# Performance work log

Hardware: AMD Instinct MI355X
Metric: run time of the kernel (lower is better)

## Reference

```python
import jax, jax.numpy as jnp
import numpy as np

A_NUM = 9
C_NUM = 20

def setup_inputs() -> dict:
    key = jax.random.key(0)
    ks = jax.random.split(key, 12)
    B, Cin, H, W = 32, 256, 56, 56
    hidden = 256
    N, M = 64, 2048
    out_ch = 5 * A_NUM + C_NUM
    features = jax.random.normal(ks[0], (B, Cin, H, W), jnp.float32)
    w1 = jax.random.normal(ks[1], (hidden, Cin), jnp.float32) * (1.0 / np.sqrt(Cin))
    b1 = jax.random.normal(ks[2], (hidden,), jnp.float32) * 0.01
    w2 = jax.random.normal(ks[3], (out_ch, hidden), jnp.float32) * (1.0 / np.sqrt(hidden))
    b2 = jax.random.normal(ks[4], (out_ch,), jnp.float32) * 0.01
    # anchor shapes (w, h), positive sizes in grid units
    anc = 1.0 + 5.0 * jax.random.uniform(ks[5], (A_NUM, 2), jnp.float32)
    # grid of cell centers
    xs = jnp.arange(W, dtype=jnp.float32) + 0.5
    ys = jnp.arange(H, dtype=jnp.float32) + 0.5
    gx, gy = jnp.meshgrid(xs, ys, indexing='xy')  # (H, W)
    grid = jnp.broadcast_to(jnp.stack([gx, gy], axis=-1)[None], (B, H, W, 2))
    # GT boxes (x1, y1, x2, y2, cls) with x1<x2, y1<y2
    x1 = jax.random.uniform(ks[6], (B, N), jnp.float32) * (W - 9.0)
    y1 = jax.random.uniform(ks[7], (B, N), jnp.float32) * (H - 9.0)
    bw = 1.0 + 7.0 * jax.random.uniform(ks[8], (B, N), jnp.float32)
    bh = 1.0 + 7.0 * jax.random.uniform(ks[9], (B, N), jnp.float32)
    cls = jax.random.randint(ks[10], (B, N), 0, C_NUM).astype(jnp.float32)
    bboxes = jnp.stack([x1, y1, x1 + bw, y1 + bh, cls], axis=-1)
    total_anchors = B * A_NUM * H * W
    pos_anchor_idx = jax.random.randint(ks[11], (M,), 0, total_anchors, jnp.int64 if jax.config.jax_enable_x64 else jnp.int32)
    neg_anchor_idx = jax.random.randint(jax.random.fold_in(key, 99), (M,), 0, total_anchors, jnp.int64 if jax.config.jax_enable_x64 else jnp.int32)
    GT_offsets = jax.random.normal(jax.random.fold_in(key, 100), (M, 4), jnp.float32) * 0.1
    return {"features": features, "w1": w1, "b1": b1, "w2": w2, "b2": b2,
            "anc": anc, "grid": grid, "bboxes": bboxes, "GT_offsets": GT_offsets,
            "pos_anchor_idx": pos_anchor_idx, "neg_anchor_idx": neg_anchor_idx}

def _generate_anchor(anc, grid):
    # grid: (B,H,W,2), anc: (A,2) -> anchors (B,A,H,W,4) as (x1,y1,x2,y2)
    g = grid[:, None]                      # (B,1,H,W,2)
    a = anc[None, :, None, None]           # (1,A,1,1,2)
    return jnp.concatenate([g - a / 2, g + a / 2], axis=-1)

def _generate_proposal_yolo(anchors, offsets):
    ctr = (anchors[..., :2] + anchors[..., 2:]) / 2
    wh = anchors[..., 2:] - anchors[..., :2]
    new_wh = wh * jnp.exp(offsets[..., 2:])
    new_ctr = ctr + offsets[..., :2]
    return jnp.concatenate([new_ctr - new_wh / 2, new_ctr + new_wh / 2], axis=-1)

def _iou(proposals, bboxes):
    # proposals (B,A,H,W,4) -> (B,AHW,4); bboxes (B,N,5) -> iou (B,AHW,N)
    B = proposals.shape[0]
    p = proposals.reshape(B, -1, 4)[:, :, None, :]   # (B,AHW,1,4)
    g = bboxes[:, None, :, :]                        # (B,1,N,5)
    ix1 = jnp.maximum(p[..., 0], g[..., 0])
    iy1 = jnp.maximum(p[..., 1], g[..., 1])
    ix2 = jnp.minimum(p[..., 2], g[..., 2])
    iy2 = jnp.minimum(p[..., 3], g[..., 3])
    inter = jnp.clip(ix2 - ix1, 0) * jnp.clip(iy2 - iy1, 0)
    gt_area = (bboxes[:, :, 2] - bboxes[:, :, 0]) * (bboxes[:, :, 3] - bboxes[:, :, 1])
    p_area = (p[..., 2] - p[..., 0]) * (p[..., 3] - p[..., 1])
    return inter / (gt_area[:, None, :] + p_area - inter)

def reference(features, w1, b1, w2, b2, anc, grid, bboxes, GT_offsets,
              pos_anchor_idx, neg_anchor_idx):
    B, _, H, W = features.shape
    A = anc.shape[0]
    M = pos_anchor_idx.shape[0]
    # PredictionNetwork (dropout in eval = identity), 1x1 convs as einsum
    x = jnp.einsum('bchw,oc->bohw', features, w1) + b1[None, :, None, None]
    x = jax.nn.leaky_relu(x, 0.01)
    x = jnp.einsum('bchw,oc->bohw', x, w2) + b2[None, :, None, None]
    anc_data = x[:, :5 * A].reshape(B, A, 5, H, W)
    class_all = x[:, 5 * A:]                               # (B,C,H,W)
    conf_all = jax.nn.sigmoid(anc_data[:, :, 0])           # (B,A,H,W)
    offsets_all = jnp.transpose(anc_data[:, :, 1:5], (0, 1, 3, 4, 2))  # (B,A,H,W,4)
    # training extraction
    conf_flat = conf_all.reshape(-1)
    conf_scores = jnp.concatenate([conf_flat[pos_anchor_idx], conf_flat[neg_anchor_idx]])[:, None]  # (2M,1)
    offsets_pos = offsets_all.reshape(-1, 4)[pos_anchor_idx]            # (M,4)
    # class scores for positive anchors: index arithmetic over (B,A,H,W)
    bi = pos_anchor_idx // (A * H * W)
    hw = pos_anchor_idx % (H * W)
    hi, wi = hw // W, hw % W
    class_pos = class_all[bi, :, hi, wi]                                # (M,C)
    # anchors -> proposals -> IoU
    anchors = _generate_anchor(anc, grid)
    proposals = _generate_proposal_yolo(anchors, offsets_all)
    iou_mat = _iou(proposals, bboxes)                                   # (B,AHW,N)
    # YOLO SSE losses
    gt_conf = jnp.concatenate([jnp.ones((M, 1), conf_scores.dtype), jnp.zeros((M, 1), conf_scores.dtype)])
    conf_loss = jnp.sum((conf_scores - gt_conf) ** 2) / (2 * M)
    reg_loss = jnp.sum((offsets_pos - GT_offsets) ** 2) / M
    total_loss = conf_loss + reg_loss
    return total_loss, iou_mat, class_pos
```

## Files before the change

kernel.cpp:

```cpp
#include <hip/hip_runtime.h>
#include <math.h>

#define B_    32
#define CIN   256
#define HID   256
#define OC    65
#define A_    9
#define H_    56
#define W_    56
#define HW    3136
#define AHW   28224
#define NBOX  64
#define M_    2048
#define CNUM  20
#define NTILE 49

#define IOU_N ((size_t)B_ * AHW * NBOX)

#define FOFF(frag) (((frag) << 3) + ((((frag) >> 3)) << 3))

typedef _Float16 half8 __attribute__((ext_vector_type(8)));
typedef float f32x16 __attribute__((ext_vector_type(16)));
typedef float f32x4  __attribute__((ext_vector_type(4)));

__device__ __forceinline__ unsigned int pkh(float a, float b) {
    _Float16 ha = (_Float16)a, hb = (_Float16)b;
    unsigned short ua = __builtin_bit_cast(unsigned short, ha);
    unsigned short ub = __builtin_bit_cast(unsigned short, hb);
    return (unsigned int)ua | ((unsigned int)ub << 16);
}

__global__ __launch_bounds__(256) void prep_kernel(
    const float* __restrict__ w1, const float* __restrict__ w2,
    _Float16* __restrict__ w1s, _Float16* __restrict__ w2s,
    float* __restrict__ loss_ws)
{
    const int f = blockIdx.x * 256 + threadIdx.x;
    if (f < 2) loss_ws[f] = 0.f;
    {
        const int e    = f & 7;
        const int lane = (f >> 3) & 63;
        const int kc   = (f >> 9) & 15;
        const int ob   = f >> 13;
        const int row  = ob * 32 + (lane & 31);
        const int k    = kc * 16 + (lane >> 5) * 8 + e;
        w1s[f] = (_Float16)w1[row * CIN + k];
    }
    if (f < 20480) {
        const int e    = f & 7;
        const int lane = (f >> 3) & 63;
        const int ks2  = (f >> 9) & 7;
        const int rt   = f >> 12;
        const int row  = rt * 16 + (lane & 15);
        const int k    = ks2 * 32 + (lane >> 4) * 8 + e;
        w2s[f] = (row < OC) ? (_Float16)w2[row * HID + k] : (_Float16)0.f;
    }
}

__global__ __launch_bounds__(256) void conv_iou_kernel(
    const float* __restrict__ features, const _Float16* __restrict__ w1s,
    const float* __restrict__ b1, const _Float16* __restrict__ w2s,
    const float* __restrict__ b2, const float* __restrict__ anc,
    const float* __restrict__ bboxes, const int* __restrict__ pos_idx,
    const int* __restrict__ neg_idx, const float* __restrict__ gt_off,
    float* __restrict__ iou_out, float* __restrict__ cls_out,
    float* __restrict__ loss_ws)
{
    __shared__ _Float16 lds_h[18432];
    __shared__ float bias_s[HID];
    __shared__ float boxs[5 * 64];
    __shared__ float red[8];

    _Float16* featAll = lds_h;
    _Float16* hidf    = lds_h;
    float*    L       = (float*)lds_h;
    float*    x2t     = L;

    const int t    = threadIdx.x;
    const int lane = t & 63;
    const int w    = t >> 6;
    const int bid  = blockIdx.x;
    const int b    = bid / NTILE;
    const int p0   = (bid - b * NTILE) * 64;
    const float* fbase = features + (size_t)b * CIN * HW + p0;

    float* WPw = L + 4416 + w * 720;

    bias_s[t] = b1[t];
    if (t < 64) {
        const float* gb = bboxes + ((size_t)b * NBOX + t) * 5;
        const float x1 = gb[0], y1 = gb[1], x2v = gb[2], y2v = gb[3];
        boxs[t] = x1; boxs[64 + t] = y1; boxs[128 + t] = x2v; boxs[192 + t] = y2v;
        boxs[256 + t] = (x2v - x1) * (y2v - y1);
    }

    const int pstage = (t & 15) * 4;
    const int kk     = (t >> 4) * 2;
    const int ksS    = kk >> 4;
    const int gS     = (kk >> 3) & 1;
    const int j0h    = kk & 7;
    const int ghalf  = lane >> 5;

#pragma unroll
    for (int hf = 0; hf < 2; ++hf) {
        float4 r0[4], r1[4];
#pragma unroll
        for (int c4 = 0; c4 < 4; ++c4) {
            const int c = hf * 4 + c4;
            r0[c4] = *(const float4*)(fbase + (size_t)(c * 32 + kk) * HW + pstage);
            r1[c4] = *(const float4*)(fbase + (size_t)(c * 32 + kk + 1) * HW + pstage);
        }
#pragma unroll
        for (int c4 = 0; c4 < 4; ++c4) {
            const int c = hf * 4 + c4;
            const float a0[4] = {r0[c4].x, r0[c4].y, r0[c4].z, r0[c4].w};
            const float a1[4] = {r1[c4].x, r1[c4].y, r1[c4].z, r1[c4].w};
#pragma unroll
            for (int e = 0; e < 4; ++e) {
                const int p     = pstage + e;
                const int lane2 = gS * 32 + (p & 31);
                const int pt    = p >> 5;
                const int frag  = c * 256 + (ksS * 2 + pt) * 64 + lane2;
                *(unsigned int*)&featAll[FOFF(frag) + j0h] = pkh(a0[e], a1[e]);
            }
        }
    }
    __syncthreads();

    f32x16 facc[2][2];
#pragma unroll
    for (int ot = 0; ot < 2; ++ot)
#pragma unroll
        for (int pt = 0; pt < 2; ++pt)
#pragma unroll
            for (int e = 0; e < 16; ++e) facc[ot][pt][e] = 0.f;

    half8 afb[2][2][2];
#pragma unroll
    for (int ks = 0; ks < 2; ++ks)
#pragma unroll
        for (int ot = 0; ot < 2; ++ot)
            afb[0][ks][ot] = *(const half8*)(w1s + ((size_t)((w * 2 + ot) * 16 + ks) * 64 + lane) * 8);

#pragma unroll
    for (int c = 0; c < 8; ++c) {
        if (c < 7) {
#pragma unroll
            for (int ks = 0; ks < 2; ++ks)
#pragma unroll
                for (int ot = 0; ot < 2; ++ot)
                    afb[(c + 1) & 1][ks][ot] =
                        *(const half8*)(w1s + ((size_t)((w * 2 + ot) * 16 + (c + 1) * 2 + ks) * 64 + lane) * 8);
        }
#pragma unroll
        for (int ks = 0; ks < 2; ++ks) {
#pragma unroll
            for (int pt = 0; pt < 2; ++pt) {
                const half8 bf = *(const half8*)&featAll[FOFF(c * 256 + (ks * 2 + pt) * 64 + lane)];
                facc[0][pt] = __builtin_amdgcn_mfma_f32_32x32x16_f16(afb[c & 1][ks][0], bf, facc[0][pt], 0, 0, 0);
                facc[1][pt] = __builtin_amdgcn_mfma_f32_32x32x16_f16(afb[c & 1][ks][1], bf, facc[1][pt], 0, 0, 0);
            }
        }
    }
    __syncthreads();

    const int col = lane & 31;
#pragma unroll
    for (int ot = 0; ot < 2; ++ot) {
        const int ks2 = w * 2 + ot;
#pragma unroll
        for (int pt = 0; pt < 2; ++pt) {
            const int pt2 = pt * 2 + (col >> 4);
            const int n15 = col & 15;
#pragma unroll
            for (int q = 0; q < 4; ++q) {
                float hv[4];
#pragma unroll
                for (int i = 0; i < 4; ++i) {
                    const int row = i + 8 * q + 4 * ghalf;
                    float v = facc[ot][pt][q * 4 + i] + bias_s[w * 64 + ot * 32 + row];
                    hv[i] = v < 0.f ? 0.01f * v : v;
                }
                const int frag = (ks2 * 4 + pt2) * 64 + (q * 16 + n15);
                *(unsigned int*)&hidf[FOFF(frag) + 4 * ghalf]     = pkh(hv[0], hv[1]);
                *(unsigned int*)&hidf[FOFF(frag) + 4 * ghalf + 2] = pkh(hv[2], hv[3]);
            }
        }
    }
    __syncthreads();

    f32x4 c2[5];
#pragma unroll
    for (int rt = 0; rt < 5; ++rt)
#pragma unroll
        for (int e = 0; e < 4; ++e) c2[rt][e] = 0.f;

    const int m16 = lane & 15;
    const int kgr = lane >> 4;

    half8 afc[2][5];
#pragma unroll
    for (int rt = 0; rt < 5; ++rt)
        afc[0][rt] = *(const half8*)(w2s + ((size_t)(rt * 8) * 64 + lane) * 8);

#pragma unroll
    for (int ks2 = 0; ks2 < 8; ++ks2) {
        if (ks2 < 7) {
#pragma unroll
            for (int rt = 0; rt < 5; ++rt)
                afc[(ks2 + 1) & 1][rt] =
                    *(const half8*)(w2s + ((size_t)(rt * 8 + ks2 + 1) * 64 + lane) * 8);
        }
        const half8 bf = *(const half8*)&hidf[FOFF((ks2 * 4 + w) * 64 + lane)];
#pragma unroll
        for (int rt = 0; rt < 5; ++rt)
            c2[rt] = __builtin_amdgcn_mfma_f32_16x16x32_f16(afc[ks2 & 1][rt], bf, c2[rt], 0, 0, 0);
    }
    __syncthreads();

    const int pxl = w * 16 + m16;
#pragma unroll
    for (int rt = 0; rt < 5; ++rt) {
#pragma unroll
        for (int r = 0; r < 4; ++r) {
            const int o2 = rt * 16 + kgr * 4 + r;
            if (o2 < OC) x2t[pxl * 69 + o2] = c2[rt][r] + b2[o2];
        }
    }
    asm volatile("" ::: "memory");

    for (int i = lane; i < A_ * 16; i += 64) {
        const int a  = i >> 4;
        const int pw = i & 15;
        const float* xr = x2t + (w * 16 + pw) * 69 + 5 * a;
        const float tx = xr[1], ty = xr[2], tw = xr[3], th = xr[4];
        const int hwg = p0 + w * 16 + pw;
        const int h   = hwg / W_;
        const int wv  = hwg - h * W_;
        const float gx = (float)wv + 0.5f;
        const float gy = (float)h + 0.5f;
        const float nw = anc[2 * a]     * __expf(tw);
        const float nh = anc[2 * a + 1] * __expf(th);
        const float cx = gx + tx, cy = gy + ty;
        WPw[i]       = cx - 0.5f * nw;
        WPw[144 + i] = cy - 0.5f * nh;
        WPw[288 + i] = cx + 0.5f * nw;
        WPw[432 + i] = cy + 0.5f * nh;
        WPw[576 + i] = nw * nh;
    }
    asm volatile("" ::: "memory");

    const int pr = lane >> 4;
    const int j0 = (lane & 15) * 4;
    float Bx1[4], By1[4], Bx2[4], By2[4], Ba[4];
#pragma unroll
    for (int e = 0; e < 4; ++e) {
        Bx1[e] = boxs[j0 + e];       By1[e] = boxs[64 + j0 + e];
        Bx2[e] = boxs[128 + j0 + e]; By2[e] = boxs[192 + j0 + e];
        Ba[e]  = boxs[256 + j0 + e];
    }
    float* ibase = iou_out + ((size_t)b * AHW + p0) * 64;
#pragma unroll 1
    for (int a = 0; a < A_; ++a) {
        float Px1[4], Py1[4], Px2[4], Py2[4], Pa[4];
#pragma unroll
        for (int q = 0; q < 4; ++q) {
            const int idx = a * 16 + q * 4 + pr;
            Px1[q] = WPw[idx];       Py1[q] = WPw[144 + idx];
            Px2[q] = WPw[288 + idx]; Py2[q] = WPw[432 + idx];
            Pa[q]  = WPw[576 + idx];
        }
#pragma unroll
        for (int q = 0; q < 4; ++q) {
            f32x4 o4;
#pragma unroll
            for (int e = 0; e < 4; ++e) {
                const float iw = fminf(Px2[q], Bx2[e]) - fmaxf(Px1[q], Bx1[e]);
                const float ih = fminf(Py2[q], By2[e]) - fmaxf(Py1[q], By1[e]);
                const float inter = fmaxf(iw, 0.f) * fmaxf(ih, 0.f);
                o4[e] = inter * __builtin_amdgcn_rcpf(Ba[e] + Pa[q] - inter);
            }
            *(f32x4*)(ibase + ((size_t)(a * HW) + w * 16 + q * 4 + pr) * 64 + j0) = o4;
        }
    }

    __syncthreads();

    float csum = 0.f, rsum = 0.f;
    for (int m = t; m < M_; m += 256) {
        const int ip = pos_idx[m];
        const int in_ = neg_idx[m];
        {
            const int bi  = ip / AHW;
            const int rr  = ip - bi * AHW;
            const int a   = rr / HW;
            const int px  = (rr - a * HW) - p0;
            if (bi == b && px >= 0 && px < 64) {
                const float* xr = x2t + px * 69;
                const float s = 1.f / (1.f + __expf(-xr[5 * a]));
                csum += (s - 1.f) * (s - 1.f);
#pragma unroll
                for (int k = 0; k < 4; ++k) {
                    const float d = xr[5 * a + 1 + k] - gt_off[m * 4 + k];
                    rsum += d * d;
                }
                float* co = cls_out + (size_t)m * CNUM;
#pragma unroll
                for (int c = 0; c < CNUM; ++c) co[c] = xr[45 + c];
            }
        }
        {
            const int bi  = in_ / AHW;
            const int rr  = in_ - bi * AHW;
            const int a   = rr / HW;
            const int px  = (rr - a * HW) - p0;
            if (bi == b && px >= 0 && px < 64) {
                const float s = 1.f / (1.f + __expf(-x2t[px * 69 + 5 * a]));
                csum += s * s;
            }
        }
    }
#pragma unroll
    for (int off = 32; off > 0; off >>= 1) {
        csum += __shfl_down(csum, off, 64);
        rsum += __shfl_down(rsum, off, 64);
    }
    if (lane == 0) { red[w] = csum; red[4 + w] = rsum; }
    __syncthreads();
    if (t == 0) {
        const float c  = red[0] + red[1] + red[2] + red[3];
        const float rg = red[4] + red[5] + red[6] + red[7];
        if (c != 0.f || rg != 0.f) {
            atomicAdd(&loss_ws[0], c);
            atomicAdd(&loss_ws[1], rg);
        }
    }
}

__global__ void finalize_kernel(const float* __restrict__ loss_ws, float* __restrict__ out0)
{
    out0[0] = loss_ws[0] / (2.f * (float)M_) + loss_ws[1] / (float)M_;
}

extern "C" void kernel_launch(void* const* d_in, const int* in_sizes, int n_in,
                              void* d_out, int out_size, void* d_ws, size_t ws_size,
                              hipStream_t stream) {
    (void)in_sizes; (void)n_in; (void)out_size; (void)ws_size;
    const float* features = (const float*)d_in[0];
    const float* w1       = (const float*)d_in[1];
    const float* b1       = (const float*)d_in[2];
    const float* w2       = (const float*)d_in[3];
    const float* b2       = (const float*)d_in[4];
    const float* anc      = (const float*)d_in[5];
    const float* bboxes   = (const float*)d_in[7];
    const float* gt_off   = (const float*)d_in[8];
    const int*   pos_idx  = (const int*)d_in[9];
    const int*   neg_idx  = (const int*)d_in[10];
    float* out = (float*)d_out;

    char* wsb = (char*)d_ws;
    _Float16* w1s  = (_Float16*)wsb;
    _Float16* w2s  = w1s + 65536;
    float* loss_ws = (float*)(wsb + 131072 + 40960);

    prep_kernel<<<256, 256, 0, stream>>>(w1, w2, w1s, w2s, loss_ws);
    conv_iou_kernel<<<B_ * NTILE, 256, 0, stream>>>(features, w1s, b1, w2s, b2,
                                                    anc, bboxes, pos_idx, neg_idx,
                                                    gt_off, out + 1,
                                                    out + 1 + IOU_N, loss_ws);
    finalize_kernel<<<1, 1, 0, stream>>>(loss_ws, out);
}
```

Measured before the change: 385.9 us.

## Bucket anchor indices per tile and process two tiles per block with prefetch

```diff
diff --git a/kernel.cpp b/kernel.cpp
--- a/kernel.cpp
+++ b/kernel.cpp
@@ -14,8 +14,18 @@
 #define M_    2048
 #define CNUM  20
 #define NTILE 49
+#define NTILES_TOT (B_ * NTILE)
+#define NSLOT 25
 
 #define IOU_N ((size_t)B_ * AHW * NBOX)
+
+#define WS_W1S   0
+#define WS_W2S   131072
+#define WS_LOSS  172032
+#define WS_PCNT  172288
+#define WS_NCNT  178560
+#define WS_PBUF  184832
+#define WS_NBUF  586240
 
 #define FOFF(frag) (((frag) << 3) + ((((frag) >> 3)) << 3))
 
@@ -30,13 +40,28 @@
     return (unsigned int)ua | ((unsigned int)ub << 16);
 }
 
+__device__ __forceinline__ void phase_barrier() {
+    __builtin_amdgcn_sched_barrier(0);
+    asm volatile("s_waitcnt lgkmcnt(0)" ::: "memory");
+    __builtin_amdgcn_s_barrier();
+    __builtin_amdgcn_sched_barrier(0);
+}
+
+__global__ __launch_bounds__(256) void zero_kernel(int* __restrict__ cnts,
+                                                   float* __restrict__ loss_ws) {
+    const int i = blockIdx.x * 256 + threadIdx.x;
+    if (i < 2 * NTILES_TOT) cnts[i] = 0;
+    if (i < 2) loss_ws[i] = 0.f;
+}
+
 __global__ __launch_bounds__(256) void prep_kernel(
     const float* __restrict__ w1, const float* __restrict__ w2,
     _Float16* __restrict__ w1s, _Float16* __restrict__ w2s,
-    float* __restrict__ loss_ws)
+    const int* __restrict__ pos_idx, const int* __restrict__ neg_idx,
+    int* __restrict__ pcnt, int* __restrict__ ncnt,
+    int* __restrict__ pbuf, int* __restrict__ nbuf)
 {
     const int f = blockIdx.x * 256 + threadIdx.x;
-    if (f < 2) loss_ws[f] = 0.f;
     {
         const int e    = f & 7;
         const int lane = (f >> 3) & 63;
@@ -55,14 +80,65 @@
         const int k    = ks2 * 32 + (lane >> 4) * 8 + e;
         w2s[f] = (row < OC) ? (_Float16)w2[row * HID + k] : (_Float16)0.f;
     }
+    if (f < 2 * M_) {
+        const int m   = f & (M_ - 1);
+        const int idx = (f < M_) ? pos_idx[m] : neg_idx[m];
+        const int bi  = idx / AHW;
+        const int rr  = idx - bi * AHW;
+        const int a   = rr / HW;
+        const int hw  = rr - a * HW;
+        const int tile = bi * NTILE + (hw >> 6);
+        const int enc  = m | (a << 11) | ((hw & 63) << 15);
+        if (f < M_) {
+            const int s = atomicAdd(&pcnt[tile], 1);
+            if (s < 64) pbuf[tile * 64 + s] = enc;
+        } else {
+            const int s = atomicAdd(&ncnt[tile], 1);
+            if (s < 64) nbuf[tile * 64 + s] = enc;
+        }
+    }
+}
+
+__device__ __forceinline__ void stage_issue(const float* __restrict__ fbase,
+                                            int kk, int pstage,
+                                            float4* __restrict__ s0,
+                                            float4* __restrict__ s1)
+{
+#pragma unroll
+    for (int c = 0; c < 8; ++c) {
+        s0[c] = *(const float4*)(fbase + (size_t)(c * 32 + kk) * HW + pstage);
+        s1[c] = *(const float4*)(fbase + (size_t)(c * 32 + kk + 1) * HW + pstage);
+    }
+}
+
+__device__ __forceinline__ void stage_store(_Float16* __restrict__ featAll,
+                                            int pstage, int ksS, int gS, int j0h,
+                                            const float4* __restrict__ s0,
+                                            const float4* __restrict__ s1)
+{
+#pragma unroll
+    for (int c = 0; c < 8; ++c) {
+        const float a0[4] = {s0[c].x, s0[c].y, s0[c].z, s0[c].w};
+        const float a1[4] = {s1[c].x, s1[c].y, s1[c].z, s1[c].w};
+#pragma unroll
+        for (int e = 0; e < 4; ++e) {
+            const int p     = pstage + e;
+            const int lane2 = gS * 32 + (p & 31);
+            const int pt    = p >> 5;
+            const int frag  = c * 256 + (ksS * 2 + pt) * 64 + lane2;
+            *(unsigned int*)&featAll[FOFF(frag) + j0h] = pkh(a0[e], a1[e]);
+        }
+    }
 }
 
 __global__ __launch_bounds__(256) void conv_iou_kernel(
     const float* __restrict__ features, const _Float16* __restrict__ w1s,
     const float* __restrict__ b1, const _Float16* __restrict__ w2s,
     const float* __restrict__ b2, const float* __restrict__ anc,
-    const float* __restrict__ bboxes, const int* __restrict__ pos_idx,
-    const int* __restrict__ neg_idx, const float* __restrict__ gt_off,
+    const float* __restrict__ bboxes,
+    const int* __restrict__ pcnt, const int* __restrict__ ncnt,
+    const int* __restrict__ pbuf, const int* __restrict__ nbuf,
+    const float* __restrict__ gt_off,
     float* __restrict__ iou_out, float* __restrict__ cls_out,
     float* __restrict__ loss_ws)
 {
@@ -80,9 +156,11 @@
     const int lane = t & 63;
     const int w    = t >> 6;
     const int bid  = blockIdx.x;
-    const int b    = bid / NTILE;
-    const int p0   = (bid - b * NTILE) * 64;
-    const float* fbase = features + (size_t)b * CIN * HW + p0;
+    const int b    = bid / NSLOT;
+    const int slot = bid - b * NSLOT;
+    const int j0t  = slot * 2;
+    const int ntiles = (slot < NSLOT - 1) ? 2 : 1;
+    const float* fb0 = features + (size_t)b * CIN * HW;
 
     float* WPw = L + 4416 + w * 720;
 
@@ -100,202 +178,192 @@
     const int gS     = (kk >> 3) & 1;
     const int j0h    = kk & 7;
     const int ghalf  = lane >> 5;
-
-#pragma unroll
-    for (int hf = 0; hf < 2; ++hf) {
-        float4 r0[4], r1[4];
-#pragma unroll
-        for (int c4 = 0; c4 < 4; ++c4) {
-            const int c = hf * 4 + c4;
-            r0[c4] = *(const float4*)(fbase + (size_t)(c * 32 + kk) * HW + pstage);
-            r1[c4] = *(const float4*)(fbase + (size_t)(c * 32 + kk + 1) * HW + pstage);
-        }
-#pragma unroll
-        for (int c4 = 0; c4 < 4; ++c4) {
-            const int c = hf * 4 + c4;
-            const float a0[4] = {r0[c4].x, r0[c4].y, r0[c4].z, r0[c4].w};
-            const float a1[4] = {r1[c4].x, r1[c4].y, r1[c4].z, r1[c4].w};
+    const int col    = lane & 31;
+    const int m16    = lane & 15;
+    const int kgr    = lane >> 4;
+    const int pr     = lane >> 4;
+    const int j0     = (lane & 15) * 4;
+
+    float Bx1[4], By1[4], Bx2[4], By2[4], Ba[4];
+
+    float4 s0[8], s1[8];
+    stage_issue(fb0 + j0t * 64, kk, pstage, s0, s1);
+
+    float csum = 0.f, rsum = 0.f;
+
+    for (int it = 0; it < ntiles; ++it) {
+        const int p0 = (j0t + it) * 64;
+
+        stage_store(featAll, pstage, ksS, gS, j0h, s0, s1);
+        phase_barrier();
+
+        if (it == 0) {
 #pragma unroll
             for (int e = 0; e < 4; ++e) {
-                const int p     = pstage + e;
-                const int lane2 = gS * 32 + (p & 31);
-                const int pt    = p >> 5;
-                const int frag  = c * 256 + (ksS * 2 + pt) * 64 + lane2;
-                *(unsigned int*)&featAll[FOFF(frag) + j0h] = pkh(a0[e], a1[e]);
-            }
-        }
-    }
-    __syncthreads();
-
-    f32x16 facc[2][2];
-#pragma unroll
-    for (int ot = 0; ot < 2; ++ot)
-#pragma unroll
-        for (int pt = 0; pt < 2; ++pt)
-#pragma unroll
-            for (int e = 0; e < 16; ++e) facc[ot][pt][e] = 0.f;
-
-    half8 afb[2][2][2];
-#pragma unroll
-    for (int ks = 0; ks < 2; ++ks)
+                Bx1[e] = boxs[j0 + e];       By1[e] = boxs[64 + j0 + e];
+                Bx2[e] = boxs[128 + j0 + e]; By2[e] = boxs[192 + j0 + e];
+                Ba[e]  = boxs[256 + j0 + e];
+            }
+        }
+
+        f32x16 facc[2][2];
 #pragma unroll
         for (int ot = 0; ot < 2; ++ot)
-            afb[0][ks][ot] = *(const half8*)(w1s + ((size_t)((w * 2 + ot) * 16 + ks) * 64 + lane) * 8);
-
-#pragma unroll
-    for (int c = 0; c < 8; ++c) {
-        if (c < 7) {
-#pragma unroll
-            for (int ks = 0; ks < 2; ++ks)
-#pragma unroll
-                for (int ot = 0; ot < 2; ++ot)
-                    afb[(c + 1) & 1][ks][ot] =
-                        *(const half8*)(w1s + ((size_t)((w * 2 + ot) * 16 + (c + 1) * 2 + ks) * 64 + lane) * 8);
-        }
-#pragma unroll
-        for (int ks = 0; ks < 2; ++ks) {
+#pragma unroll
+            for (int pt = 0; pt < 2; ++pt)
+#pragma unroll
+                for (int e = 0; e < 16; ++e) facc[ot][pt][e] = 0.f;
+
+        half8 afb[2][2][2];
+#pragma unroll
+        for (int ks = 0; ks < 2; ++ks)
+#pragma unroll
+            for (int ot = 0; ot < 2; ++ot)
+                afb[0][ks][ot] = *(const half8*)(w1s + ((size_t)((w * 2 + ot) * 16 + ks) * 64 + lane) * 8);
+
+#pragma unroll
+        for (int c = 0; c < 8; ++c) {
+            if (c < 7) {
+#pragma unroll
+                for (int ks = 0; ks < 2; ++ks)
+#pragma unroll
+                    for (int ot = 0; ot < 2; ++ot)
+                        afb[(c + 1) & 1][ks][ot] =
+                            *(const half8*)(w1s + ((size_t)((w * 2 + ot) * 16 + (c + 1) * 2 + ks) * 64 + lane) * 8);
+            }
+#pragma unroll
+            for (int ks = 0; ks < 2; ++ks) {
+#pragma unroll
+                for (int pt = 0; pt < 2; ++pt) {
+                    const half8 bf = *(const half8*)&featAll[FOFF(c * 256 + (ks * 2 + pt) * 64 + lane)];
+                    facc[0][pt] = __builtin_amdgcn_mfma_f32_32x32x16_f16(afb[c & 1][ks][0], bf, facc[0][pt], 0, 0, 0);
+                    facc[1][pt] = __builtin_amdgcn_mfma_f32_32x32x16_f16(afb[c & 1][ks][1], bf, facc[1][pt], 0, 0, 0);
+                }
+            }
+        }
+        phase_barrier();
+
+#pragma unroll
+        for (int ot = 0; ot < 2; ++ot) {
+            const int ks2 = w * 2 + ot;
 #pragma unroll
             for (int pt = 0; pt < 2; ++pt) {
-                const half8 bf = *(const half8*)&featAll[FOFF(c * 256 + (ks * 2 + pt) * 64 + lane)];
-                facc[0][pt] = __builtin_amdgcn_mfma_f32_32x32x16_f16(afb[c & 1][ks][0], bf, facc[0][pt], 0, 0, 0);
-                facc[1][pt] = __builtin_amdgcn_mfma_f32_32x32x16_f16(afb[c & 1][ks][1], bf, facc[1][pt], 0, 0, 0);
-            }
-        }
-    }
-    __syncthreads();
-
-    const int col = lane & 31;
-#pragma unroll
-    for (int ot = 0; ot < 2; ++ot) {
-        const int ks2 = w * 2 + ot;
-#pragma unroll
-        for (int pt = 0; pt < 2; ++pt) {
-            const int pt2 = pt * 2 + (col >> 4);
-            const int n15 = col & 15;
+                const int pt2 = pt * 2 + (col >> 4);
+                const int n15 = col & 15;
+#pragma unroll
+                for (int q = 0; q < 4; ++q) {
+                    float hv[4];
+#pragma unroll
+                    for (int i = 0; i < 4; ++i) {
+                        const int row = i + 8 * q + 4 * ghalf;
+                        float v = facc[ot][pt][q * 4 + i] + bias_s[w * 64 + ot * 32 + row];
+                        hv[i] = v < 0.f ? 0.01f * v : v;
+                    }
+                    const int frag = (ks2 * 4 + pt2) * 64 + (q * 16 + n15);
+                    *(unsigned int*)&hidf[FOFF(frag) + 4 * ghalf]     = pkh(hv[0], hv[1]);
+                    *(unsigned int*)&hidf[FOFF(frag) + 4 * ghalf + 2] = pkh(hv[2], hv[3]);
+                }
+            }
+        }
+        phase_barrier();
+
+        f32x4 c2[5];
+#pragma unroll
+        for (int rt = 0; rt < 5; ++rt)
+#pragma unroll
+            for (int e = 0; e < 4; ++e) c2[rt][e] = 0.f;
+
+        half8 afc[2][5];
+#pragma unroll
+        for (int rt = 0; rt < 5; ++rt)
+            afc[0][rt] = *(const half8*)(w2s + ((size_t)(rt * 8) * 64 + lane) * 8);
+
+#pragma unroll
+        for (int ks2 = 0; ks2 < 8; ++ks2) {
+            if (ks2 < 7) {
+#pragma unroll
+                for (int rt = 0; rt < 5; ++rt)
+                    afc[(ks2 + 1) & 1][rt] =
+                        *(const half8*)(w2s + ((size_t)(rt * 8 + ks2 + 1) * 64 + lane) * 8);
+            }
+            const half8 bf = *(const half8*)&hidf[FOFF((ks2 * 4 + w) * 64 + lane)];
+#pragma unroll
+            for (int rt = 0; rt < 5; ++rt)
+                c2[rt] = __builtin_amdgcn_mfma_f32_16x16x32_f16(afc[ks2 & 1][rt], bf, c2[rt], 0, 0, 0);
+        }
+
+        if (it + 1 < ntiles)
+            stage_issue(fb0 + (p0 + 64), kk, pstage, s0, s1);
+
+        phase_barrier();
+
+        const int pxl = w * 16 + m16;
+#pragma unroll
+        for (int rt = 0; rt < 5; ++rt) {
+#pragma unroll
+            for (int r = 0; r < 4; ++r) {
+                const int o2 = rt * 16 + kgr * 4 + r;
+                if (o2 < OC) x2t[pxl * 69 + o2] = c2[rt][r] + b2[o2];
+            }
+        }
+        asm volatile("" ::: "memory");
+
+        for (int i = lane; i < A_ * 16; i += 64) {
+            const int a  = i >> 4;
+            const int pw = i & 15;
+            const float* xr = x2t + (w * 16 + pw) * 69 + 5 * a;
+            const float tx = xr[1], ty = xr[2], tw = xr[3], th = xr[4];
+            const int hwg = p0 + w * 16 + pw;
+            const int h   = hwg / W_;
+            const int wv  = hwg - h * W_;
+            const float gx = (float)wv + 0.5f;
+            const float gy = (float)h + 0.5f;
+            const float nw = anc[2 * a]     * __expf(tw);
+            const float nh = anc[2 * a + 1] * __expf(th);
+            const float cx = gx + tx, cy = gy + ty;
+            WPw[i]       = cx - 0.5f * nw;
+            WPw[144 + i] = cy - 0.5f * nh;
+            WPw[288 + i] = cx + 0.5f * nw;
+            WPw[432 + i] = cy + 0.5f * nh;
+            WPw[576 + i] = nw * nh;
+        }
+        asm volatile("" ::: "memory");
+
+        float* ibase = iou_out + ((size_t)b * AHW + p0) * 64;
+#pragma unroll 1
+        for (int a = 0; a < A_; ++a) {
+            float Px1[4], Py1[4], Px2[4], Py2[4], Pa[4];
 #pragma unroll
             for (int q = 0; q < 4; ++q) {
-                float hv[4];
-#pragma unroll
-                for (int i = 0; i < 4; ++i) {
-                    const int row = i + 8 * q + 4 * ghalf;
-                    float v = facc[ot][pt][q * 4 + i] + bias_s[w * 64 + ot * 32 + row];
-                    hv[i] = v < 0.f ? 0.01f * v : v;
+                const int idx = a * 16 + q * 4 + pr;
+                Px1[q] = WPw[idx];       Py1[q] = WPw[144 + idx];
+                Px2[q] = WPw[288 + idx]; Py2[q] = WPw[432 + idx];
+                Pa[q]  = WPw[576 + idx];
+            }
+#pragma unroll
+            for (int q = 0; q < 4; ++q) {
+                f32x4 o4;
+#pragma unroll
+                for (int e = 0; e < 4; ++e) {
+                    const float iw = fminf(Px2[q], Bx2[e]) - fmaxf(Px1[q], Bx1[e]);
+                    const float ih = fminf(Py2[q], By2[e]) - fmaxf(Py1[q], By1[e]);
+                    const float inter = fmaxf(iw, 0.f) * fmaxf(ih, 0.f);
+                    o4[e] = inter * __builtin_amdgcn_rcpf(Ba[e] + Pa[q] - inter);
                 }
-                const int frag = (ks2 * 4 + pt2) * 64 + (q * 16 + n15);
-                *(unsigned int*)&hidf[FOFF(frag) + 4 * ghalf]     = pkh(hv[0], hv[1]);
-                *(unsigned int*)&hidf[FOFF(frag) + 4 * ghalf + 2] = pkh(hv[2], hv[3]);
-            }
-        }
-    }
-    __syncthreads();
-
-    f32x4 c2[5];
-#pragma unroll
-    for (int rt = 0; rt < 5; ++rt)
-#pragma unroll
-        for (int e = 0; e < 4; ++e) c2[rt][e] = 0.f;
-
-    const int m16 = lane & 15;
-    const int kgr = lane >> 4;
-
-    half8 afc[2][5];
-#pragma unroll
-    for (int rt = 0; rt < 5; ++rt)
-        afc[0][rt] = *(const half8*)(w2s + ((size_t)(rt * 8) * 64 + lane) * 8);
-
-#pragma unroll
-    for (int ks2 = 0; ks2 < 8; ++ks2) {
-        if (ks2 < 7) {
-#pragma unroll
-            for (int rt = 0; rt < 5; ++rt)
-                afc[(ks2 + 1) & 1][rt] =
-                    *(const half8*)(w2s + ((size_t)(rt * 8 + ks2 + 1) * 64 + lane) * 8);
-        }
-        const half8 bf = *(const half8*)&hidf[FOFF((ks2 * 4 + w) * 64 + lane)];
-#pragma unroll
-        for (int rt = 0; rt < 5; ++rt)
-            c2[rt] = __builtin_amdgcn_mfma_f32_16x16x32_f16(afc[ks2 & 1][rt], bf, c2[rt], 0, 0, 0);
-    }
-    __syncthreads();
-
-    const int pxl = w * 16 + m16;
-#pragma unroll
-    for (int rt = 0; rt < 5; ++rt) {
-#pragma unroll
-        for (int r = 0; r < 4; ++r) {
-            const int o2 = rt * 16 + kgr * 4 + r;
-            if (o2 < OC) x2t[pxl * 69 + o2] = c2[rt][r] + b2[o2];
-        }
-    }
-    asm volatile("" ::: "memory");
-
-    for (int i = lane; i < A_ * 16; i += 64) {
-        const int a  = i >> 4;
-        const int pw = i & 15;
-        const float* xr = x2t + (w * 16 + pw) * 69 + 5 * a;
-        const float tx = xr[1], ty = xr[2], tw = xr[3], th = xr[4];
-        const int hwg = p0 + w * 16 + pw;
-        const int h   = hwg / W_;
-        const int wv  = hwg - h * W_;
-        const float gx = (float)wv + 0.5f;
-        const float gy = (float)h + 0.5f;
-        const float nw = anc[2 * a]     * __expf(tw);
-        const float nh = anc[2 * a + 1] * __expf(th);
-        const float cx = gx + tx, cy = gy + ty;
-        WPw[i]       = cx - 0.5f * nw;
-        WPw[144 + i] = cy - 0.5f * nh;
-        WPw[288 + i] = cx + 0.5f * nw;
-        WPw[432 + i] = cy + 0.5f * nh;
-        WPw[576 + i] = nw * nh;
-    }
-    asm volatile("" ::: "memory");
-
-    const int pr = lane >> 4;
-    const int j0 = (lane & 15) * 4;
-    float Bx1[4], By1[4], Bx2[4], By2[4], Ba[4];
-#pragma unroll
-    for (int e = 0; e < 4; ++e) {
-        Bx1[e] = boxs[j0 + e];       By1[e] = boxs[64 + j0 + e];
-        Bx2[e] = boxs[128 + j0 + e]; By2[e] = boxs[192 + j0 + e];
-        Ba[e]  = boxs[256 + j0 + e];
-    }
-    float* ibase = iou_out + ((size_t)b * AHW + p0) * 64;
-#pragma unroll 1
-    for (int a = 0; a < A_; ++a) {
-        float Px1[4], Py1[4], Px2[4], Py2[4], Pa[4];
-#pragma unroll
-        for (int q = 0; q < 4; ++q) {
-            const int idx = a * 16 + q * 4 + pr;
-            Px1[q] = WPw[idx];       Py1[q] = WPw[144 + idx];
-            Px2[q] = WPw[288 + idx]; Py2[q] = WPw[432 + idx];
-            Pa[q]  = WPw[576 + idx];
-        }
-#pragma unroll
-        for (int q = 0; q < 4; ++q) {
-            f32x4 o4;
-#pragma unroll
-            for (int e = 0; e < 4; ++e) {
-                const float iw = fminf(Px2[q], Bx2[e]) - fmaxf(Px1[q], Bx1[e]);
-                const float ih = fminf(Py2[q], By2[e]) - fmaxf(Py1[q], By1[e]);
-                const float inter = fmaxf(iw, 0.f) * fmaxf(ih, 0.f);
-                o4[e] = inter * __builtin_amdgcn_rcpf(Ba[e] + Pa[q] - inter);
-            }
-            *(f32x4*)(ibase + ((size_t)(a * HW) + w * 16 + q * 4 + pr) * 64 + j0) = o4;
-        }
-    }
-
-    __syncthreads();
-
-    float csum = 0.f, rsum = 0.f;
-    for (int m = t; m < M_; m += 256) {
-        const int ip = pos_idx[m];
-        const int in_ = neg_idx[m];
+                *(f32x4*)(ibase + ((size_t)(a * HW) + w * 16 + q * 4 + pr) * 64 + j0) = o4;
+            }
+        }
+
+        phase_barrier();
+
         {
-            const int bi  = ip / AHW;
-            const int rr  = ip - bi * AHW;
-            const int a   = rr / HW;
-            const int px  = (rr - a * HW) - p0;
-            if (bi == b && px >= 0 && px < 64) {
+            const int bidt = b * NTILE + j0t + it;
+            int np = pcnt[bidt]; np = np > 64 ? 64 : np;
+            for (int i = t; i < np; i += 256) {
+                const int e  = pbuf[bidt * 64 + i];
+                const int m  = e & 2047;
+                const int a  = (e >> 11) & 15;
+                const int px = (e >> 15) & 63;
                 const float* xr = x2t + px * 69;
                 const float s = 1.f / (1.f + __expf(-xr[5 * a]));
                 csum += (s - 1.f) * (s - 1.f);
@@ -308,18 +376,18 @@
 #pragma unroll
                 for (int c = 0; c < CNUM; ++c) co[c] = xr[45 + c];
             }
-        }
-        {
-            const int bi  = in_ / AHW;
-            const int rr  = in_ - bi * AHW;
-            const int a   = rr / HW;
-            const int px  = (rr - a * HW) - p0;
-            if (bi == b && px >= 0 && px < 64) {
+            int nn = ncnt[bidt]; nn = nn > 64 ? 64 : nn;
+            for (int i = t; i < nn; i += 256) {
+                const int e  = nbuf[bidt * 64 + i];
+                const int a  = (e >> 11) & 15;
+                const int px = (e >> 15) & 63;
                 const float s = 1.f / (1.f + __expf(-x2t[px * 69 + 5 * a]));
                 csum += s * s;
             }
         }
-    }
+        phase_barrier();
+    }
+
 #pragma unroll
     for (int off = 32; off > 0; off >>= 1) {
         csum += __shfl_down(csum, off, 64);
@@ -359,13 +427,19 @@
     float* out = (float*)d_out;
 
     char* wsb = (char*)d_ws;
-    _Float16* w1s  = (_Float16*)wsb;
-    _Float16* w2s  = w1s + 65536;
-    float* loss_ws = (float*)(wsb + 131072 + 40960);
-
-    prep_kernel<<<256, 256, 0, stream>>>(w1, w2, w1s, w2s, loss_ws);
-    conv_iou_kernel<<<B_ * NTILE, 256, 0, stream>>>(features, w1s, b1, w2s, b2,
-                                                    anc, bboxes, pos_idx, neg_idx,
+    _Float16* w1s  = (_Float16*)(wsb + WS_W1S);
+    _Float16* w2s  = (_Float16*)(wsb + WS_W2S);
+    float* loss_ws = (float*)(wsb + WS_LOSS);
+    int*   pcnt    = (int*)(wsb + WS_PCNT);
+    int*   ncnt    = (int*)(wsb + WS_NCNT);
+    int*   pbuf    = (int*)(wsb + WS_PBUF);
+    int*   nbuf    = (int*)(wsb + WS_NBUF);
+
+    zero_kernel<<<13, 256, 0, stream>>>(pcnt, loss_ws);
+    prep_kernel<<<256, 256, 0, stream>>>(w1, w2, w1s, w2s, pos_idx, neg_idx,
+                                         pcnt, ncnt, pbuf, nbuf);
+    conv_iou_kernel<<<B_ * NSLOT, 256, 0, stream>>>(features, w1s, b1, w2s, b2,
+                                                    anc, bboxes, pcnt, ncnt, pbuf, nbuf,
                                                     gt_off, out + 1,
                                                     out + 1 + IOU_N, loss_ws);
     finalize_kernel<<<1, 1, 0, stream>>>(loss_ws, out);
```

Result: slower. 432.3 us (+12.0%).
